# Kernel tuning notes

Measured on AMD Instinct MI355X. Metric: run time of the kernel, lower is better.

The kernel has to match this reference:

```python
import jax, jax.numpy as jnp
import numpy as np
from jax import lax

B, T, IN, H, DIM = 128, 1024, 64, 128, 64


def setup_inputs() -> dict:
    key = jax.random.key(0)
    ks = jax.random.split(key, 14)
    s = 0.05
    return {
        "x": jax.random.normal(ks[0], (B, T, IN), jnp.float32),
        "is_init": jax.random.randint(ks[1], (B, T, 1), 0, 2).astype(bool),
        "hx": jax.random.normal(ks[2], (B, H), jnp.float32),
        # MLP: Linear(IN,128) + ELU, Linear(128,128) + ELU
        "W1": jax.random.normal(ks[3], (128, IN), jnp.float32) * s,
        "b1": jnp.zeros((128,), jnp.float32),
        "W2": jax.random.normal(ks[4], (128, 128), jnp.float32) * s,
        "b2": jnp.zeros((128,), jnp.float32),
        # GRU params (torch layout: [3H, in] with gate order r,z,n)
        "W_ih": jax.random.normal(ks[5], (3 * H, 128), jnp.float32) * s,
        "b_ih": jnp.zeros((3 * H,), jnp.float32),
        "W_hh": jax.random.normal(ks[6], (3 * H, H), jnp.float32) * s,
        "b_hh": jnp.zeros((3 * H,), jnp.float32),
        # output head Linear(128, DIM)
        "W_out": jax.random.normal(ks[7], (DIM, 128), jnp.float32) * s,
        "b_out": jnp.zeros((DIM,), jnp.float32),
    }


def _gru_with_reset(xg, init_mask, h0, W_hh, b_hh):
    # xg: [T,B,3H] precomputed input-side gates; init_mask: [T,B,1] float
    def step(h, inp):
        xg_t, m_t = inp
        h = h * (1.0 - m_t)                       # reset hidden where is_init
        hg = h @ W_hh.T + b_hh                    # [B,3H]
        xr, xz, xn = jnp.split(xg_t, 3, axis=-1)
        hr, hz, hn = jnp.split(hg, 3, axis=-1)
        r = jax.nn.sigmoid(xr + hr)
        z = jax.nn.sigmoid(xz + hz)
        n = jnp.tanh(xn + r * hn)
        h_new = (1.0 - z) * n + z * h
        return h_new, h_new

    hT, ys = lax.scan(step, h0, (xg, init_mask))
    return ys, hT


def reference(x, is_init, hx, W1, b1, W2, b2, W_ih, b_ih, W_hh, b_hh, W_out, b_out):
    # MLP (ELU activations)
    h = jax.nn.elu(x @ W1.T + b1)
    h = jax.nn.elu(h @ W2.T + b2)                 # [B,T,128]
    # precompute input-side gate projections for all timesteps (one big GEMM)
    xg = h @ W_ih.T + b_ih                        # [B,T,3H]
    xg_t = jnp.transpose(xg, (1, 0, 2))           # [T,B,3H]
    m_t = jnp.transpose(is_init.astype(x.dtype), (1, 0, 2))  # [T,B,1]
    ys, hT = _gru_with_reset(xg_t, m_t, hx, W_hh, b_hh)
    y = jnp.transpose(ys, (1, 0, 2))              # [B,T,H]
    out = y @ W_out.T + b_out                     # [B,T,DIM]
    return out, hT
```

## Files before the change

### kernel.cpp

```cpp
#include <hip/hip_runtime.h>


#define T_SZ 1024

typedef __attribute__((ext_vector_type(8))) short short8;
typedef __attribute__((ext_vector_type(4))) float f32x4;
typedef unsigned long long u64;
typedef unsigned int uint32;

__device__ __forceinline__ unsigned short f2b(float f){
  return __builtin_bit_cast(unsigned short, (__bf16)f);
}
__device__ __forceinline__ float b2f(unsigned int hs){
  unsigned int u = hs << 16;
  return __builtin_bit_cast(float, u);
}
__device__ __forceinline__ float rcp_f(float x){ return __builtin_amdgcn_rcpf(x); }
__device__ __forceinline__ float elu(float v){ return v > 0.f ? v : __expf(v) - 1.f; }
__device__ __forceinline__ float sigm(float x){ return rcp_f(1.f + __expf(-x)); }
__device__ __forceinline__ float tanh_fast(float x){
  x = fminf(fmaxf(x, -15.f), 15.f);
  float e = __expf(-2.f * x);
  return (1.f - e) * rcp_f(1.f + e);
}
#define MFMA16(a,b,c) __builtin_amdgcn_mfma_f32_16x16x32_bf16(a, b, c, 0, 0, 0)


__global__ __launch_bounds__(512) void wprep(
    const float* __restrict__ Whh, const float* __restrict__ W1,
    const float* __restrict__ W2,  const float* __restrict__ Wih,
    uint4* __restrict__ wtab)
{
  int rec = blockIdx.x*512 + threadIdx.x;
  if(rec >= 15360) return;
  const float* p;
  if(rec < 6144){
    int q = rec & 3, n_ = (rec >> 2) & 127, ks = (rec >> 9) & 3, gt = rec >> 11;
    p = Whh + (size_t)(n_ + 128*gt)*128 + ks*32 + q*8;
  } else if(rec < 7168){
    int r = rec - 6144;
    int q = r & 3, n_ = (r >> 2) & 127, ks = r >> 9;
    p = W1 + (size_t)n_*64 + ks*32 + q*8;
  } else if(rec < 9216){
    int r = rec - 7168;
    int q = r & 3, n_ = (r >> 2) & 127, ks = r >> 9;
    p = W2 + (size_t)n_*128 + ks*32 + q*8;
  } else {
    int r = rec - 9216;
    int q = r & 3, n_ = (r >> 2) & 127, ks = (r >> 9) & 3, gt = r >> 11;
    p = Wih + (size_t)(n_ + 128*gt)*128 + ks*32 + q*8;
  }
  uint4 o;
  o.x = (uint32)f2b(p[0]) | ((uint32)f2b(p[1]) << 16);
  o.y = (uint32)f2b(p[2]) | ((uint32)f2b(p[3]) << 16);
  o.z = (uint32)f2b(p[4]) | ((uint32)f2b(p[5]) << 16);
  o.w = (uint32)f2b(p[6]) | ((uint32)f2b(p[7]) << 16);
  wtab[rec] = o;
}

__global__ __launch_bounds__(512) void seg_build(const int* __restrict__ ii, uint32* C){
  __shared__ uint32 lh[1024];
  __shared__ uint32 lbase[1024];
  __shared__ uint32 ssum[512];
  __shared__ uint32 sbase;
  uint32* segs = C + 4096;
  const int tid = threadIdx.x;
  const int wv = tid >> 6, lane = tid & 63;
  const int b = blockIdx.x*8 + wv;

  for(int i = tid; i < 1024; i += 512) lh[i] = 0u;
  __syncthreads();

  u64 bal[16], mb[16];
  #pragma unroll
  for(int c=0;c<16;c++){
    int t = c*64 + lane;
    int m = ii[b*T_SZ + t];
    mb[c]  = __ballot(m != 0);
    bal[c] = __ballot((m != 0) || (t == 0));
  }
  int fsA[16]; int nx = T_SZ;
  #pragma unroll
  for(int c=15;c>=0;c--){ fsA[c]=nx; if(bal[c]) nx = c*64 + __builtin_ctzll(bal[c]); }

  int lenA[16], tA[16], rkA[16];
  #pragma unroll
  for(int c=0;c<16;c++){
    lenA[c] = 0;
    if((bal[c] >> lane) & 1ull){
      int t = c*64 + lane;
      u64 hi = (lane < 63) ? (bal[c] >> (lane+1)) : 0ull;
      int nxt = hi ? (t + 1 + __builtin_ctzll(hi)) : fsA[c];
      int len = nxt - t;
      int rst = (int)((mb[c] >> lane) & 1ull);
      len -= rst; t += rst;
      if(len > 0){
        lenA[c] = len; tA[c] = t;
        rkA[c] = (int)atomicAdd(&lh[1024 - len], 1u);
      }
    }
  }
  __syncthreads();

  uint32 c0 = lh[2*tid], c1 = lh[2*tid+1];
  ssum[tid] = c0 + c1;
  __syncthreads();
  #pragma unroll
  for(int off=1; off<512; off<<=1){
    uint32 v = (tid >= off) ? ssum[tid-off] : 0u;
    __syncthreads();
    ssum[tid] += v;
    __syncthreads();
  }
  uint32 excl = tid ? ssum[tid-1] : 0u;
  lbase[2*tid]   = excl;
  lbase[2*tid+1] = excl + c0;
  uint32 total = ssum[511];
  uint32 padded = (total + 15u) & ~15u;
  if(tid == 0){
    sbase = atomicAdd(&C[2], padded);
    atomicAdd(&C[1], padded >> 4);
  }
  __syncthreads();
  const uint32 base = sbase;

  #pragma unroll
  for(int c=0;c<16;c++){
    if(lenA[c] > 0){
      uint32 slot = base + lbase[1024 - lenA[c]] + (uint32)rkA[c];
      segs[slot] = ((uint32)b << 21) | ((uint32)tA[c] << 11) | (uint32)lenA[c];
    }
  }
  for(uint32 i = total + tid; i < padded; i += 512) segs[base + i] = 0u;
}

__global__ __launch_bounds__(512) void mlp2(
    const float* __restrict__ x,
    const uint4* __restrict__ wtab,
    const float* __restrict__ b1, const float* __restrict__ b2,
    unsigned short* __restrict__ h2)
{
  __shared__ __align__(16) char smem[35840];
  unsigned short* xs  = (unsigned short*)smem;
  unsigned short* h1l = (unsigned short*)(smem + 18432);
  const int tid = threadIdx.x;
  const int wv = tid >> 6, l = tid & 63, quad = l >> 4, col = l & 15;
  const int n = 16*wv + col;

  short8 w1f[2], w2f[4];
  #pragma unroll
  for(int ks=0; ks<2; ks++)
    w1f[ks] = __builtin_bit_cast(short8, wtab[6144 + (ks*128 + n)*4 + quad]);
  #pragma unroll
  for(int ks=0; ks<4; ks++)
    w2f[ks] = __builtin_bit_cast(short8, wtab[7168 + (ks*128 + n)*4 + quad]);
  const float b1v = b1[n], b2v = b2[n];

  const int srow = tid >> 5, sk = tid & 31;

  for(int tile = blockIdx.x; tile < 2048; tile += gridDim.x){
    const int g = tile & 7, t0 = (tile >> 3) * 4;
    {
      const float* src = x + (size_t)(16*g + srow)*(T_SZ*64) + (size_t)t0*64;
      #pragma unroll
      for(int j=0; j<2; j++){
        int s = sk + 32*j;
        float4 v = ((const float4*)src)[s];
        int tt = s >> 4, k = (s & 15) * 4;
        unsigned short* dst = xs + (tt*16 + srow)*72 + k;
        dst[0]=f2b(v.x); dst[1]=f2b(v.y); dst[2]=f2b(v.z); dst[3]=f2b(v.w);
      }
    }
    __syncthreads();
    #pragma unroll
    for(int tt=0; tt<4; tt++){
      f32x4 acc = {b1v, b1v, b1v, b1v};
      #pragma unroll
      for(int ks=0; ks<2; ks++){
        short8 a = *(const short8*)&xs[(tt*16 + col)*72 + ks*32 + quad*8];
        acc = MFMA16(a, w1f[ks], acc);
      }
      #pragma unroll
      for(int r=0; r<4; r++)
        h1l[(tt*16 + quad*4 + r)*136 + n] = f2b(elu(acc[r]));
    }
    __syncthreads();
    #pragma unroll
    for(int tt=0; tt<4; tt++){
      f32x4 acc = {b2v, b2v, b2v, b2v};
      #pragma unroll
      for(int ks=0; ks<4; ks++){
        short8 a = *(const short8*)&h1l[(tt*16 + col)*136 + ks*32 + quad*8];
        acc = MFMA16(a, w2f[ks], acc);
      }
      const int t = t0 + tt;
      #pragma unroll
      for(int r=0; r<4; r++){
        int row = quad*4 + r;
        h2[((size_t)(t*8 + g)*16 + row)*128 + n] = f2b(elu(acc[r]));
      }
    }
    __syncthreads();
  }
}

__global__ __launch_bounds__(512) void xgproj(
    const unsigned short* h2, const int* __restrict__ ii,
    const uint4* __restrict__ wtab,
    const float* __restrict__ bih, const float* __restrict__ bhh,
    unsigned short* __restrict__ xg, unsigned short* ys,
    float* __restrict__ hT)
{
  __shared__ __align__(16) unsigned short h2l[4*16*136];
  __shared__ int iil[64];
  const int tid = threadIdx.x;
  const int wv = tid >> 6, l = tid & 63, quad = l >> 4, col = l & 15;
  const int n = 16*wv + col;

  short8 wif[3][4];
  #pragma unroll
  for(int gt=0; gt<3; gt++){
    #pragma unroll
    for(int ks=0; ks<4; ks++)
      wif[gt][ks] = __builtin_bit_cast(short8, wtab[9216 + ((gt*4 + ks)*128 + n)*4 + quad]);
  }
  float bihv[3], bhhv[3];
  #pragma unroll
  for(int gt=0; gt<3; gt++){ bihv[gt] = bih[n + 128*gt]; bhhv[gt] = bhh[n + 128*gt]; }

  for(int tile = blockIdx.x; tile < 2048; tile += gridDim.x){
    const int g = tile & 7, t0 = (tile >> 3) * 4;
    {
      const int w = tid >> 3, j = tid & 7;
      const int tt = w >> 4, row = w & 15;
      const unsigned short* src = h2 + ((size_t)((t0 + tt)*8 + g)*16 + row)*128 + j*16;
      unsigned short* dst = &h2l[(tt*16 + row)*136 + j*16];
      #pragma unroll
      for(int i2=0; i2<4; i2++)
        *(u64*)(dst + i2*4) = *(const u64*)(src + i2*4);
    }
    if(tid < 64) iil[tid] = ii[(16*g + (tid & 15))*T_SZ + t0 + (tid >> 4)];
    __syncthreads();

    uint32 xgo[4];
    #pragma unroll
    for(int r=0; r<4; r++)
      xgo[r] = (((uint32)(16*g + quad*4 + r) << 10) + (uint32)t0) * 384u + (uint32)n;
    #pragma unroll
    for(int tt=0; tt<4; tt++){
      f32x4 a0 = {bihv[0], bihv[0], bihv[0], bihv[0]};
      f32x4 a1 = {bihv[1], bihv[1], bihv[1], bihv[1]};
      f32x4 a2 = {bihv[2], bihv[2], bihv[2], bihv[2]};
      #pragma unroll
      for(int ks=0; ks<4; ks++){
        short8 a = *(const short8*)&h2l[(tt*16 + col)*136 + ks*32 + quad*8];
        a0 = MFMA16(a, wif[0][ks], a0);
        a1 = MFMA16(a, wif[1][ks], a1);
        a2 = MFMA16(a, wif[2][ks], a2);
      }
      const int t = t0 + tt;
      #pragma unroll
      for(int r=0; r<4; r++){
        int row = quad*4 + r;
        if(iil[tt*16 + row] != 0){
          float rr = sigm(a0[r] + bhhv[0]);
          float zz = sigm(a1[r] + bhhv[1]);
          float nn = tanh_fast(a2[r] + rr*bhhv[2]);
          float h1 = (1.f - zz)*nn;
          ys[((size_t)(t*8 + g)*16 + row)*128 + n] = f2b(h1);
          if(t == T_SZ-1)
            hT[(16*g + row)*128 + n] = h1;
        } else {
          unsigned short* p = xg + xgo[r] + (uint32)(tt*384);
          p[0]   = f2b(a0[r]);
          p[128] = f2b(a1[r]);
          p[256] = f2b(a2[r]);
        }
      }
    }
    __syncthreads();
  }
}

__global__ __launch_bounds__(512) void gru_seg_scan(
    const unsigned short* __restrict__ xg,
    const float* __restrict__ hx,
    const uint4* __restrict__ wbf, const float* __restrict__ bhh,
    const uint32* __restrict__ C,
    unsigned short* __restrict__ ys, float* __restrict__ hT)
{
  __shared__ unsigned short hl[2][16*136];
  __shared__ unsigned short xbuf[2][16*388];
  __shared__ int srb[16], srt[16], srlen[16];
  const uint32 ntile = C[1];

  const int tid = threadIdx.x;
  const int wv = tid >> 6, l = tid & 63, quad = l >> 4, col = l & 15;
  const int nidx = 16*wv + col;
  const int frow = tid >> 5, fk = tid & 31;
  const uint32* segs = C + 4096;

  short8 whf[3][4];
  float bhv[3];
  #pragma unroll
  for(int gt=0; gt<3; gt++){
    bhv[gt] = bhh[nidx + 128*gt];
    #pragma unroll
    for(int ks=0; ks<4; ks++){
      uint4 w = wbf[((gt*4 + ks)*128 + nidx)*4 + quad];
      whf[gt][ks] = __builtin_bit_cast(short8, w);
    }
  }

  for(int p = 0; p < 4; p++){
    __syncthreads();
    const uint32 tile = (uint32)((p >> 1) * 2080)
                      + ((p & 1) ? (uint32)(2079 - (int)blockIdx.x) : blockIdx.x);
    if(tile >= ntile) continue;

    if(tid < 16){
      uint32 w = segs[16*tile + (uint32)tid];
      srb[tid] = (int)(w >> 21);
      srt[tid] = (int)((w >> 11) & 1023u);
      srlen[tid] = (int)(w & 2047u);
    }
    __syncthreads();
    const int maxlen = srlen[0];
    const int fb = srb[frow], ft = srt[frow], fl = srlen[frow];

    {
      if(fl > 0){
        if(ft == 0){
          float4 hv = *(const float4*)(hx + fb*128 + fk*4);
          unsigned short* d = &hl[0][frow*136 + fk*4];
          d[0]=f2b(hv.x); d[1]=f2b(hv.y); d[2]=f2b(hv.z); d[3]=f2b(hv.w);
        } else {
          u64 hv = *(const u64*)(ys + ((size_t)((ft-1)*8 + (fb>>4))*16 + (fb&15))*128 + fk*4);
          *(u64*)&hl[0][frow*136 + fk*4] = hv;
        }
      } else {
        *(u64*)&hl[0][frow*136 + fk*4] = 0ull;
      }
    }
    {
      const unsigned short* src = xg + ((size_t)fb*T_SZ + ft)*384;
      unsigned short* xb = &xbuf[0][frow*388];
      #pragma unroll
      for(int i2=0; i2<3; i2++)
        *(u64*)(xb + i2*128 + fk*4) = *(const u64*)(src + i2*128 + fk*4);
    }
    __syncthreads();

    float hreg[4];
    #pragma unroll
    for(int r=0; r<4; r++){
      int row = quad*4 + r;
      hreg[r] = (srlen[row] > 0 && srt[row] == 0)
                  ? hx[srb[row]*128 + nidx]
                  : b2f(hl[0][row*136 + nidx]);
    }

    int cur = 0;
    for(int i=0; i<maxlen; i++){
      __syncthreads();
      short8 af[4];
      #pragma unroll
      for(int ks=0; ks<4; ks++)
        af[ks] = *(const short8*)&hl[cur][col*136 + ks*32 + quad*8];
      f32x4 ar = {bhv[0], bhv[0], bhv[0], bhv[0]};
      f32x4 az = {bhv[1], bhv[1], bhv[1], bhv[1]};
      f32x4 an = {bhv[2], bhv[2], bhv[2], bhv[2]};
      #pragma unroll
      for(int ks=0; ks<4; ks++){
        ar = MFMA16(af[ks], whf[0][ks], ar);
        az = MFMA16(af[ks], whf[1][ks], az);
        an = MFMA16(af[ks], whf[2][ks], an);
      }
      u64 p0, p1, p2;
      {
        int tc = (i+1 < fl) ? i+1 : (fl > 0 ? fl-1 : 0);
        const unsigned short* src = xg + ((size_t)fb*T_SZ + (ft + tc))*384;
        p0 = *(const u64*)(src +       fk*4);
        p1 = *(const u64*)(src + 128 + fk*4);
        p2 = *(const u64*)(src + 256 + fk*4);
      }
      if(i >= 1 && i <= fl){
        int t = ft + i - 1;
        u64 hv = *(const u64*)&hl[cur][frow*136 + fk*4];
        *(u64*)(ys + ((size_t)(t*8 + (fb>>4))*16 + (fb&15))*128 + fk*4) = hv;
        if(i == fl && ft + fl == T_SZ){
          #pragma unroll
          for(int j=0; j<4; j++)
            hT[fb*128 + fk*4 + j] = b2f(hl[cur][frow*136 + fk*4 + j]);
        }
      }
      const unsigned short* xb = &xbuf[cur][0];
      #pragma unroll
      for(int r=0; r<4; r++){
        int row = quad*4 + r;
        float xrv = b2f(xb[row*388 +       nidx]);
        float xzv = b2f(xb[row*388 + 128 + nidx]);
        float xnv = b2f(xb[row*388 + 256 + nidx]);
        float rr = sigm(xrv + ar[r]);
        float zz = sigm(xzv + az[r]);
        float nn = tanh_fast(xnv + rr*an[r]);
        float hnew = (1.f - zz)*nn + zz*hreg[r];
        hreg[r] = hnew;
        hl[cur^1][row*136 + nidx] = f2b(hnew);
      }
      {
        unsigned short* xb2 = &xbuf[cur^1][frow*388];
        *(u64*)(xb2 +       fk*4) = p0;
        *(u64*)(xb2 + 128 + fk*4) = p1;
        *(u64*)(xb2 + 256 + fk*4) = p2;
      }
      cur ^= 1;
    }
    __syncthreads();
    if(maxlen >= 1 && fl == maxlen){
      int t = ft + maxlen - 1;
      u64 hv = *(const u64*)&hl[cur][frow*136 + fk*4];
      *(u64*)(ys + ((size_t)(t*8 + (fb>>4))*16 + (fb&15))*128 + fk*4) = hv;
      if(ft + fl == T_SZ){
        #pragma unroll
        for(int j=0; j<4; j++)
          hT[fb*128 + fk*4 + j] = b2f(hl[cur][frow*136 + fk*4 + j]);
      }
    }
  }
}

__global__ __launch_bounds__(256) void out_gemm(
    const unsigned short* __restrict__ ys,
    const float* __restrict__ Wout, const float* __restrict__ bout,
    float* __restrict__ outp)
{
  const int tid = threadIdx.x;
  const int wv = tid >> 6, l = tid & 63, quad = l >> 4, col = l & 15;
  const int n = 16*wv + col;
  short8 wof[4];
  #pragma unroll
  for(int ks=0; ks<4; ks++){
    const float* p = Wout + n*128 + ks*32 + quad*8;
    const float4* q = (const float4*)p;
    float4 u0 = q[0], u1 = q[1];
    short8 v;
    v[0]=(short)f2b(u0.x); v[1]=(short)f2b(u0.y); v[2]=(short)f2b(u0.z); v[3]=(short)f2b(u0.w);
    v[4]=(short)f2b(u1.x); v[5]=(short)f2b(u1.y); v[6]=(short)f2b(u1.z); v[7]=(short)f2b(u1.w);
    wof[ks] = v;
  }
  const float bov = bout[n];
  for(int tile = blockIdx.x; tile < 8192; tile += gridDim.x){
    const int t = tile >> 3, g = tile & 7;
    const unsigned short* yt = ys + (size_t)tile * 16 * 128;
    f32x4 acc = {bov, bov, bov, bov};
    #pragma unroll
    for(int ks=0; ks<4; ks++){
      short8 a = *(const short8*)&yt[col*128 + ks*32 + quad*8];
      acc = MFMA16(a, wof[ks], acc);
    }
    #pragma unroll
    for(int r=0; r<4; r++)
      outp[(size_t)(16*g + quad*4 + r)*(T_SZ*64) + (size_t)t*64 + n] = acc[r];
  }
}

extern "C" void kernel_launch(void* const* d_in, const int* in_sizes, int n_in,
                              void* d_out, int out_size, void* d_ws, size_t ws_size,
                              hipStream_t stream)
{
  const float* x    = (const float*)d_in[0];
  const int*   ii   = (const int*)  d_in[1];
  const float* hx   = (const float*)d_in[2];
  const float* W1   = (const float*)d_in[3];
  const float* b1   = (const float*)d_in[4];
  const float* W2   = (const float*)d_in[5];
  const float* b2   = (const float*)d_in[6];
  const float* Wih  = (const float*)d_in[7];
  const float* bih  = (const float*)d_in[8];
  const float* Whh  = (const float*)d_in[9];
  const float* bhh  = (const float*)d_in[10];
  const float* Wout = (const float*)d_in[11];
  const float* bout = (const float*)d_in[12];

  float* outp = (float*)d_out;
  float* hT   = outp + (size_t)128 * T_SZ * 64;
  uint32* C   = (uint32*)d_out;
  uint4* wtab = (uint4*)((char*)d_out + (1u<<20));

  unsigned short* xg = (unsigned short*)d_ws;
  unsigned short* ys = (unsigned short*)((char*)d_ws + 100663296ull);

  hipMemsetAsync(C, 0, 64, stream);
  wprep      <<<dim3(30),   dim3(512),  0, stream>>>(Whh, W1, W2, Wih, wtab);
  seg_build  <<<dim3(16),   dim3(512),  0, stream>>>(ii, C);
  mlp2       <<<dim3(1024), dim3(512),  0, stream>>>(x, wtab, b1, b2, ys);
  xgproj     <<<dim3(1024), dim3(512),  0, stream>>>(ys, ii, wtab, bih, bhh, xg, ys, hT);
  gru_seg_scan<<<dim3(1040),dim3(512),  0, stream>>>(xg, hx, wtab, bhh, C, ys, hT);
  out_gemm   <<<dim3(2048), dim3(256),  0, stream>>>(ys, Wout, bout, outp);
}
```

Before: 231.2 us.

## Pipeline GRU xg loads via triple-buffered async global_load_lds and one tile per block

The GRU segment scan now stages input-gate rows into LDS with asynchronous global_load_lds into a three-deep ring, issuing loads two steps ahead. A manual vmcnt wait plus s_barrier replaces the per-step __syncthreads, which should hide global latency behind the MFMA and gate math. Each block now handles a single tile, launched over 4160 blocks, instead of looping over four tiles in a balanced order. This drops the hand-tuned load-balancing pairing and relies on the hardware scheduler. It also depends on hand-counted vmcnt values being correct.

```diff
diff --git a/kernel.cpp b/kernel.cpp
--- a/kernel.cpp
+++ b/kernel.cpp
@@ -290,9 +290,11 @@
     unsigned short* __restrict__ ys, float* __restrict__ hT)
 {
   __shared__ unsigned short hl[2][16*136];
-  __shared__ unsigned short xbuf[2][16*388];
+  __shared__ __align__(16) unsigned short xbuf[3][16*392];
   __shared__ int srb[16], srt[16], srlen[16];
   const uint32 ntile = C[1];
+  const uint32 tile = blockIdx.x;
+  if(tile >= ntile) return;
 
   const int tid = threadIdx.x;
   const int wv = tid >> 6, l = tid & 63, quad = l >> 4, col = l & 15;
@@ -312,120 +314,117 @@
     }
   }
 
-  for(int p = 0; p < 4; p++){
-    __syncthreads();
-    const uint32 tile = (uint32)((p >> 1) * 2080)
-                      + ((p & 1) ? (uint32)(2079 - (int)blockIdx.x) : blockIdx.x);
-    if(tile >= ntile) continue;
-
-    if(tid < 16){
-      uint32 w = segs[16*tile + (uint32)tid];
-      srb[tid] = (int)(w >> 21);
-      srt[tid] = (int)((w >> 11) & 1023u);
-      srlen[tid] = (int)(w & 2047u);
-    }
-    __syncthreads();
-    const int maxlen = srlen[0];
-    const int fb = srb[frow], ft = srt[frow], fl = srlen[frow];
-
-    {
-      if(fl > 0){
-        if(ft == 0){
-          float4 hv = *(const float4*)(hx + fb*128 + fk*4);
-          unsigned short* d = &hl[0][frow*136 + fk*4];
-          d[0]=f2b(hv.x); d[1]=f2b(hv.y); d[2]=f2b(hv.z); d[3]=f2b(hv.w);
-        } else {
-          u64 hv = *(const u64*)(ys + ((size_t)((ft-1)*8 + (fb>>4))*16 + (fb&15))*128 + fk*4);
-          *(u64*)&hl[0][frow*136 + fk*4] = hv;
-        }
-      } else {
-        *(u64*)&hl[0][frow*136 + fk*4] = 0ull;
-      }
-    }
-    {
-      const unsigned short* src = xg + ((size_t)fb*T_SZ + ft)*384;
-      unsigned short* xb = &xbuf[0][frow*388];
-      #pragma unroll
-      for(int i2=0; i2<3; i2++)
-        *(u64*)(xb + i2*128 + fk*4) = *(const u64*)(src + i2*128 + fk*4);
-    }
-    __syncthreads();
-
-    float hreg[4];
-    #pragma unroll
-    for(int r=0; r<4; r++){
-      int row = quad*4 + r;
-      hreg[r] = (srlen[row] > 0 && srt[row] == 0)
-                  ? hx[srb[row]*128 + nidx]
-                  : b2f(hl[0][row*136 + nidx]);
-    }
-
-    int cur = 0;
-    for(int i=0; i<maxlen; i++){
-      __syncthreads();
-      short8 af[4];
-      #pragma unroll
-      for(int ks=0; ks<4; ks++)
-        af[ks] = *(const short8*)&hl[cur][col*136 + ks*32 + quad*8];
-      f32x4 ar = {bhv[0], bhv[0], bhv[0], bhv[0]};
-      f32x4 az = {bhv[1], bhv[1], bhv[1], bhv[1]};
-      f32x4 an = {bhv[2], bhv[2], bhv[2], bhv[2]};
-      #pragma unroll
-      for(int ks=0; ks<4; ks++){
-        ar = MFMA16(af[ks], whf[0][ks], ar);
-        az = MFMA16(af[ks], whf[1][ks], az);
-        an = MFMA16(af[ks], whf[2][ks], an);
-      }
-      u64 p0, p1, p2;
-      {
-        int tc = (i+1 < fl) ? i+1 : (fl > 0 ? fl-1 : 0);
-        const unsigned short* src = xg + ((size_t)fb*T_SZ + (ft + tc))*384;
-        p0 = *(const u64*)(src +       fk*4);
-        p1 = *(const u64*)(src + 128 + fk*4);
-        p2 = *(const u64*)(src + 256 + fk*4);
-      }
-      if(i >= 1 && i <= fl){
-        int t = ft + i - 1;
-        u64 hv = *(const u64*)&hl[cur][frow*136 + fk*4];
-        *(u64*)(ys + ((size_t)(t*8 + (fb>>4))*16 + (fb&15))*128 + fk*4) = hv;
-        if(i == fl && ft + fl == T_SZ){
-          #pragma unroll
-          for(int j=0; j<4; j++)
-            hT[fb*128 + fk*4 + j] = b2f(hl[cur][frow*136 + fk*4 + j]);
-        }
-      }
-      const unsigned short* xb = &xbuf[cur][0];
-      #pragma unroll
-      for(int r=0; r<4; r++){
-        int row = quad*4 + r;
-        float xrv = b2f(xb[row*388 +       nidx]);
-        float xzv = b2f(xb[row*388 + 128 + nidx]);
-        float xnv = b2f(xb[row*388 + 256 + nidx]);
-        float rr = sigm(xrv + ar[r]);
-        float zz = sigm(xzv + az[r]);
-        float nn = tanh_fast(xnv + rr*an[r]);
-        float hnew = (1.f - zz)*nn + zz*hreg[r];
-        hreg[r] = hnew;
-        hl[cur^1][row*136 + nidx] = f2b(hnew);
-      }
-      {
-        unsigned short* xb2 = &xbuf[cur^1][frow*388];
-        *(u64*)(xb2 +       fk*4) = p0;
-        *(u64*)(xb2 + 128 + fk*4) = p1;
-        *(u64*)(xb2 + 256 + fk*4) = p2;
-      }
-      cur ^= 1;
-    }
-    __syncthreads();
-    if(maxlen >= 1 && fl == maxlen){
-      int t = ft + maxlen - 1;
+  if(tid < 16){
+    uint32 w = segs[16*tile + (uint32)tid];
+    srb[tid] = (int)(w >> 21);
+    srt[tid] = (int)((w >> 11) & 1023u);
+    srlen[tid] = (int)(w & 2047u);
+  }
+  __syncthreads();
+  const int maxlen = srlen[0];
+  const int fb = srb[frow], ft = srt[frow], fl = srlen[frow];
+
+  auto stage = [&](int buf, int tstep){
+    #pragma unroll
+    for(int c=0; c<6; c++){
+      int gc = wv*6 + c;
+      int r  = gc / 3, part = gc - r*3;
+      int sl = srlen[r];
+      int tc = (tstep < sl) ? tstep : (sl > 0 ? sl - 1 : 0);
+      const unsigned short* src = xg
+          + ((size_t)(srb[r]*T_SZ + srt[r] + tc))*384 + part*128 + l*2;
+      char* dst = (char*)&xbuf[buf][0] + r*784 + part*256;
+      __builtin_amdgcn_global_load_lds(
+          (const __attribute__((address_space(1))) void*)src,
+          (__attribute__((address_space(3))) void*)dst, 4, 0, 0);
+    }
+  };
+
+  if(fl > 0){
+    if(ft == 0){
+      float4 hv = *(const float4*)(hx + fb*128 + fk*4);
+      unsigned short* d = &hl[0][frow*136 + fk*4];
+      d[0]=f2b(hv.x); d[1]=f2b(hv.y); d[2]=f2b(hv.z); d[3]=f2b(hv.w);
+    } else {
+      u64 hv = *(const u64*)(ys + ((size_t)((ft-1)*8 + (fb>>4))*16 + (fb&15))*128 + fk*4);
+      *(u64*)&hl[0][frow*136 + fk*4] = hv;
+    }
+  } else {
+    *(u64*)&hl[0][frow*136 + fk*4] = 0ull;
+  }
+  stage(0, 0);
+  stage(1, 1);
+  __syncthreads();
+
+  float hreg[4];
+  #pragma unroll
+  for(int r=0; r<4; r++){
+    int row = quad*4 + r;
+    hreg[r] = (srlen[row] > 0 && srt[row] == 0)
+                ? hx[srb[row]*128 + nidx]
+                : b2f(hl[0][row*136 + nidx]);
+  }
+
+  int cur = 0;
+  int xc  = 0;
+  int xs3 = 2;
+  for(int i=0; i<maxlen; i++){
+    if(i >= 1){
+      asm volatile("s_waitcnt vmcnt(6) lgkmcnt(0)" ::: "memory");
+      __builtin_amdgcn_s_barrier();
+      __builtin_amdgcn_sched_barrier(0);
+    }
+    if(i >= 1 && i <= fl){
+      int t = ft + i - 1;
       u64 hv = *(const u64*)&hl[cur][frow*136 + fk*4];
       *(u64*)(ys + ((size_t)(t*8 + (fb>>4))*16 + (fb&15))*128 + fk*4) = hv;
-      if(ft + fl == T_SZ){
+      if(i == fl && ft + fl == T_SZ){
         #pragma unroll
         for(int j=0; j<4; j++)
           hT[fb*128 + fk*4 + j] = b2f(hl[cur][frow*136 + fk*4 + j]);
       }
+    }
+    stage(xs3, i + 2);
+    short8 af[4];
+    #pragma unroll
+    for(int ks=0; ks<4; ks++)
+      af[ks] = *(const short8*)&hl[cur][col*136 + ks*32 + quad*8];
+    f32x4 ar = {bhv[0], bhv[0], bhv[0], bhv[0]};
+    f32x4 az = {bhv[1], bhv[1], bhv[1], bhv[1]};
+    f32x4 an = {bhv[2], bhv[2], bhv[2], bhv[2]};
+    #pragma unroll
+    for(int ks=0; ks<4; ks++){
+      ar = MFMA16(af[ks], whf[0][ks], ar);
+      az = MFMA16(af[ks], whf[1][ks], az);
+      an = MFMA16(af[ks], whf[2][ks], an);
+    }
+    const unsigned short* xb = &xbuf[xc][0];
+    #pragma unroll
+    for(int r=0; r<4; r++){
+      int row = quad*4 + r;
+      float xrv = b2f(xb[row*392 +       nidx]);
+      float xzv = b2f(xb[row*392 + 128 + nidx]);
+      float xnv = b2f(xb[row*392 + 256 + nidx]);
+      float rr = sigm(xrv + ar[r]);
+      float zz = sigm(xzv + az[r]);
+      float nn = tanh_fast(xnv + rr*an[r]);
+      float hnew = (1.f - zz)*nn + zz*hreg[r];
+      hreg[r] = hnew;
+      hl[cur^1][row*136 + nidx] = f2b(hnew);
+    }
+    cur ^= 1;
+    xc  = (xc  == 2) ? 0 : xc  + 1;
+    xs3 = (xs3 == 2) ? 0 : xs3 + 1;
+  }
+  __syncthreads();
+  if(maxlen >= 1 && fl == maxlen){
+    int t = ft + maxlen - 1;
+    u64 hv = *(const u64*)&hl[cur][frow*136 + fk*4];
+    *(u64*)(ys + ((size_t)(t*8 + (fb>>4))*16 + (fb&15))*128 + fk*4) = hv;
+    if(ft + fl == T_SZ){
+      #pragma unroll
+      for(int j=0; j<4; j++)
+        hT[fb*128 + fk*4 + j] = b2f(hl[cur][frow*136 + fk*4 + j]);
     }
   }
 }
@@ -496,6 +495,6 @@
   seg_build  <<<dim3(16),   dim3(512),  0, stream>>>(ii, C);
   mlp2       <<<dim3(1024), dim3(512),  0, stream>>>(x, wtab, b1, b2, ys);
   xgproj     <<<dim3(1024), dim3(512),  0, stream>>>(ys, ii, wtab, bih, bhh, xg, ys, hT);
-  gru_seg_scan<<<dim3(1040),dim3(512),  0, stream>>>(xg, hx, wtab, bhh, C, ys, hT);
+  gru_seg_scan<<<dim3(4160),dim3(512),  0, stream>>>(xg, hx, wtab, bhh, C, ys, hT);
   out_gemm   <<<dim3(2048), dim3(256),  0, stream>>>(ys, Wout, bout, outp);
 }
```

Measured after the change: 248.0 us. +7.3%, slower.
